# Optimization experiments

Measured on AMD Instinct MI355X. Metric: run time of the kernel, lower is better.

The kernel has to match this reference:

```python
import jax, jax.numpy as jnp
import numpy as np
import math

B, C, T = 4, 512, 2048
LN_EPS = 1e-5

def setup_inputs() -> dict:
    key = jax.random.key(0)
    ks = jax.random.split(key, 12)
    s = 1.0 / math.sqrt(C)
    inp = {
        'feat': jax.random.normal(ks[0], (B, C, T), dtype=jnp.float32),
        'Wq': jax.random.normal(ks[1], (C, C), dtype=jnp.float32) * s,
        'bq': jax.random.normal(ks[2], (C,), dtype=jnp.float32) * s,
        'Wk': jax.random.normal(ks[3], (C, C), dtype=jnp.float32) * s,
        'bk': jax.random.normal(ks[4], (C,), dtype=jnp.float32) * s,
        'Wv': jax.random.normal(ks[5], (C, C), dtype=jnp.float32) * s,
        'bv': jax.random.normal(ks[6], (C,), dtype=jnp.float32) * s,
        'Ws': jax.random.normal(ks[7], (C, C), dtype=jnp.float32) * s,
        'bs': jax.random.normal(ks[8], (C,), dtype=jnp.float32) * s,
        'Wl': jax.random.normal(ks[9], (C,), dtype=jnp.float32) * s,
        'bl': jax.random.normal(ks[10], (1,), dtype=jnp.float32) * s,
    }
    return inp

def reference(feat, Wq, bq, Wk, bk, Wv, bv, Ws, bs, Wl, bl):
    d = feat.shape[1]
    # 1x1 Conv1d == per-position linear over channels. feat: [B,C,T]
    value = jnp.einsum('oc,bct->bto', Wv, feat) + bv          # [B,T,C]
    query = jnp.einsum('oc,bct->bto', Wq, feat) + bq          # [B,T,C]
    key_  = jnp.einsum('oc,bct->bct', Wk, feat) + bk[:, None] # [B,C,T]
    f = jnp.einsum('btc,bcs->bts', query, key_) / math.sqrt(d)
    f = jax.nn.softmax(f, axis=2)                             # [B,T,T]
    y = jnp.einsum('bts,bsc->btc', f, value)                  # [B,T,C]
    f_score = jax.nn.sigmoid(jnp.einsum('btc,c->bt', y, Wl) + bl[0])
    z = jnp.einsum('bts,bsc->btc', 1.0 - f, value)            # [B,T,C]
    b_score = 1.0 - jax.nn.sigmoid(jnp.einsum('btc,c->bt', z, Wl) + bl[0])
    f_score = (f_score + b_score) / 2.0
    y_ct = jnp.einsum('oc,btc->bot', Ws, y) + bs[:, None]     # smooth conv, [B,C,T]
    out = feat + y_ct
    # LayerNorm over (C, T) jointly, default affine (weight=1, bias=0)
    mu = jnp.mean(out, axis=(1, 2), keepdims=True)
    var = jnp.mean(jnp.square(out - mu), axis=(1, 2), keepdims=True)
    out = (out - mu) * jax.lax.rsqrt(var + LN_EPS)
    return out, f_score
```

## Files before the change

kernel.cpp:

```cpp
#include <hip/hip_runtime.h>
#include <hip/hip_bf16.h>

#define BB 4
#define CC 512
#define TT 2048
static constexpr long CT  = (long)CC * TT;
static constexpr long TC  = (long)TT * CC;
static constexpr long TTT = (long)TT * TT;
static constexpr float SM_SCALE = 0.04419417382415922f;

typedef __bf16 bf16;
typedef __attribute__((ext_vector_type(8))) __bf16 bf16x8;
typedef __attribute__((ext_vector_type(4))) __bf16 bf16x4;
typedef __attribute__((ext_vector_type(4))) float f32x4;

__device__ __forceinline__ void load_lds16(const bf16* g, bf16* l)
{
    __builtin_amdgcn_global_load_lds(
        (const __attribute__((address_space(1))) void*)g,
        (__attribute__((address_space(3))) void*)l, 16, 0, 0);
}

template <int TM, int TN, int WR, int WC, int BK>
struct Core {
    static constexpr int THREADS = WR * WC * 64;
    static constexpr int MI = TM / (WR * 16);
    static constexpr int NI = TN / (WC * 16);
    static constexpr int CPR = BK / 8;
    static constexpr int RSH = (BK == 64) ? 3 : 2;
    static constexpr int CMASK = CPR - 1;
    static constexpr int CHUNKS = (TM + TN) * CPR;
    static constexpr int ACH = TM * CPR;
    static constexpr int CPT = CHUNKS / THREADS;
    static_assert(CPT * THREADS == CHUNKS, "chunk divisibility");

    __device__ static __forceinline__ void run(
        const bf16* __restrict__ Ab, const bf16* __restrict__ Bb,
        int K, int m0, int n0, bf16* As, bf16* Bs, f32x4 (&acc)[MI][NI])
    {
        const int tid  = threadIdx.x;
        const int lane = tid & 63;
        const int wid  = tid >> 6;
        const int wr = (wid / WC) * (MI * 16);
        const int wc = (wid % WC) * (NI * 16);
        const int lm = lane & 15;
        const int lq = lane >> 4;
        for (int k0 = 0; k0 < K; k0 += BK) {
#pragma unroll
            for (int i = 0; i < CPT; ++i) {
                int c = tid + i * THREADS;
                if (c < ACH) {
                    int row = c >> RSH;
                    int gc  = (c & CMASK) ^ (row & CMASK);
                    load_lds16(Ab + (long)(m0 + row) * K + k0 + gc * 8, As + c * 8);
                } else {
                    int d = c - ACH;
                    int row = d >> RSH;
                    int gc  = (d & CMASK) ^ (row & CMASK);
                    load_lds16(Bb + (long)(n0 + row) * K + k0 + gc * 8, Bs + d * 8);
                }
            }
            __syncthreads();
#pragma unroll
            for (int ks = 0; ks < BK / 32; ++ks) {
                bf16x8 af[MI], bfr[NI];
#pragma unroll
                for (int i = 0; i < MI; ++i) {
                    int ar = wr + i * 16 + lm;
                    int cc = (ks * 4 + lq) ^ (ar & CMASK);
                    af[i] = *(const bf16x8*)(As + ar * BK + cc * 8);
                }
#pragma unroll
                for (int i = 0; i < NI; ++i) {
                    int br = wc + i * 16 + lm;
                    int cc = (ks * 4 + lq) ^ (br & CMASK);
                    bfr[i] = *(const bf16x8*)(Bs + br * BK + cc * 8);
                }
#pragma unroll
                for (int mi = 0; mi < MI; ++mi)
#pragma unroll
                    for (int ni = 0; ni < NI; ++ni)
                        acc[mi][ni] = __builtin_amdgcn_mfma_f32_16x16x32_bf16(
                            af[mi], bfr[ni], acc[mi][ni], 0, 0, 0);
            }
            __syncthreads();
        }
    }
};

struct CoreQV {
    static constexpr int THREADS = 512;
    static constexpr int MI = 2;
    static constexpr int NI = 4;
    static constexpr int BK = 64;
    static constexpr int CPR = 8, RSH = 3, CMASK = 7;
    static constexpr int ACH = 128 * 8;
    static constexpr int CHUNKS = 256 * 8;
    static constexpr int CPT = CHUNKS / THREADS;

    __device__ static __forceinline__ void run(
        const bf16* __restrict__ Ab, const bf16* __restrict__ Bq,
        const bf16* __restrict__ Bv,
        int m0, bf16* As, bf16* Bs, f32x4 (&acc)[MI][NI])
    {
        const int tid  = threadIdx.x;
        const int lane = tid & 63;
        const int wid  = tid >> 6;
        const int wr = (wid / 2) * 32;
        const int wc = (wid % 2) * 64;
        const int lm = lane & 15;
        const int lq = lane >> 4;
        for (int k0 = 0; k0 < 512; k0 += BK) {
#pragma unroll
            for (int i = 0; i < CPT; ++i) {
                int c = tid + i * THREADS;
                if (c < ACH) {
                    int row = c >> RSH;
                    int gc  = (c & CMASK) ^ (row & CMASK);
                    load_lds16(Ab + (long)(m0 + row) * 512 + k0 + gc * 8, As + c * 8);
                } else {
                    int d = c - ACH;
                    int row = d >> RSH;
                    int gc  = (d & CMASK) ^ (row & CMASK);
                    const bf16* src = (row < 64)
                        ? Bq + (long)row * 512
                        : Bv + (long)(row - 64) * 512;
                    load_lds16(src + k0 + gc * 8, Bs + d * 8);
                }
            }
            __syncthreads();
#pragma unroll
            for (int ks = 0; ks < 2; ++ks) {
                bf16x8 af[MI], bfr[NI];
#pragma unroll
                for (int i = 0; i < MI; ++i) {
                    int ar = wr + i * 16 + lm;
                    int cc = (ks * 4 + lq) ^ (ar & CMASK);
                    af[i] = *(const bf16x8*)(As + ar * BK + cc * 8);
                }
#pragma unroll
                for (int i = 0; i < NI; ++i) {
                    int br = wc + i * 16 + lm;
                    int cc = (ks * 4 + lq) ^ (br & CMASK);
                    bfr[i] = *(const bf16x8*)(Bs + br * BK + cc * 8);
                }
#pragma unroll
                for (int mi = 0; mi < MI; ++mi)
#pragma unroll
                    for (int ni = 0; ni < NI; ++ni)
                        acc[mi][ni] = __builtin_amdgcn_mfma_f32_16x16x32_bf16(
                            af[mi], bfr[ni], acc[mi][ni], 0, 0, 0);
            }
            __syncthreads();
        }
    }
};

__global__ __launch_bounds__(512)
void gemm_qv_kernel(const bf16* __restrict__ featT, const bf16* __restrict__ Wq_bf,
                    const bf16* __restrict__ Wv_bf, bf16* __restrict__ Qb,
                    bf16* __restrict__ Vt, const float* __restrict__ bq,
                    const float* __restrict__ bv, const float* __restrict__ wkc,
                    const float* __restrict__ bk, float* __restrict__ qb)
{
    __shared__ bf16 As[128 * 64];
    __shared__ bf16 Bs[128 * 64];
    const int rb = blockIdx.z;
    const int m0 = blockIdx.y * 128;
    const int ng = blockIdx.x;
    const long wofs = (long)(ng * 64) * 512;
    f32x4 acc[2][4] = {};
    CoreQV::run(featT + (long)rb * TC, Wq_bf + wofs, Wv_bf + wofs, m0, As, Bs, acc);

    const int lane = threadIdx.x & 63, wid = threadIdx.x >> 6;
    const int wr = (wid / 2) * 32;
    const bool isV = wid & 1;
    const int lm = lane & 15, lq = lane >> 4;

    if (isV) {
        bf16* outV = Vt + (long)rb * CT;
#pragma unroll
        for (int mi = 0; mi < 2; ++mi)
#pragma unroll
            for (int ni = 0; ni < 4; ++ni) {
                int n = ng * 64 + ni * 16 + lm;
                float bn = bv[n];
                int mb = m0 + wr + mi * 16 + lq * 4;
                bf16x4 pk;
#pragma unroll
                for (int r = 0; r < 4; ++r) pk[r] = (bf16)(acc[mi][ni][r] + bn);
                *(bf16x4*)(outV + (long)n * TT + mb) = pk;
            }
    } else {
        bf16* out = Qb + (long)rb * TC;
        float* qbb = qb + (long)rb * TT;
        float rs[2][4] = {};
#pragma unroll
        for (int mi = 0; mi < 2; ++mi)
#pragma unroll
            for (int ni = 0; ni < 4; ++ni) {
                int n = ng * 64 + ni * 16 + lm;
                float bn = bq[n], wn = wkc[n], kn = bk[n];
#pragma unroll
                for (int r = 0; r < 4; ++r) {
                    int m = m0 + wr + mi * 16 + lq * 4 + r;
                    float v = acc[mi][ni][r] + bn;
                    rs[mi][r] += v * kn;
                    out[(long)m * 512 + n] = (bf16)(v * wn);
                }
            }
#pragma unroll
        for (int mi = 0; mi < 2; ++mi)
#pragma unroll
            for (int r = 0; r < 4; ++r) {
                float s = rs[mi][r];
                s += __shfl_xor(s, 1, 64); s += __shfl_xor(s, 2, 64);
                s += __shfl_xor(s, 4, 64); s += __shfl_xor(s, 8, 64);
                if (lm == 0)
                    atomicAdd(qbb + m0 + wr + mi * 16 + lq * 4 + r, s);
            }
    }
}

using CS = Core<128, 128, 4, 2, 64>;
__global__ __launch_bounds__(512)
void gemm_s_kernel(const bf16* __restrict__ Qb, const bf16* __restrict__ featT,
                   bf16* __restrict__ S, const float* __restrict__ qb,
                   float* __restrict__ rsum)
{
    __shared__ bf16 As[128 * 64];
    __shared__ bf16 Bs[128 * 64];
    const int id = blockIdx.x;
    const int xcd = id & 7, s = id >> 3;
    const int bz = xcd >> 1;
    const int n0 = (s & 15) * 128;
    const int m0 = (((xcd & 1) << 3) + (s >> 4)) * 128;
    f32x4 acc[CS::MI][CS::NI] = {};
    CS::run(Qb + (long)bz * TC, featT + (long)bz * TC, 512, m0, n0, As, Bs, acc);

    const int lane = threadIdx.x & 63, wid = threadIdx.x >> 6;
    const int wr = (wid >> 1) * 32, wc = (wid & 1) * 64;
    const int lm = lane & 15, lq = lane >> 4;
    bf16* out = S + (long)bz * TTT;
    const float* qbb = qb + (long)bz * TT;
    float* rsb = rsum + (long)bz * TT;
    float rp[2][4] = {};
#pragma unroll
    for (int mi = 0; mi < 2; ++mi)
#pragma unroll
        for (int ni = 0; ni < 4; ++ni)
#pragma unroll
            for (int r = 0; r < 4; ++r) {
                int m = m0 + wr + mi * 16 + lq * 4 + r;
                int n = n0 + wc + ni * 16 + lm;
                float p = __expf((acc[mi][ni][r] + qbb[m]) * SM_SCALE);
                out[(long)m * 2048 + n] = (bf16)p;
                rp[mi][r] += p;
            }
#pragma unroll
    for (int mi = 0; mi < 2; ++mi)
#pragma unroll
        for (int r = 0; r < 4; ++r) {
            float s2 = rp[mi][r];
            s2 += __shfl_xor(s2, 1, 64); s2 += __shfl_xor(s2, 2, 64);
            s2 += __shfl_xor(s2, 4, 64); s2 += __shfl_xor(s2, 8, 64);
            if (lm == 0)
                atomicAdd(rsb + m0 + wr + mi * 16 + lq * 4 + r, s2);
        }
}

using CY = Core<128, 64, 4, 2, 64>;
__global__ __launch_bounds__(512)
void gemm_y_kernel(const bf16* __restrict__ S, const bf16* __restrict__ Vt,
                   bf16* __restrict__ Yb, const float* __restrict__ Wl,
                   const float* __restrict__ rsum, float* __restrict__ u)
{
    __shared__ bf16 As[128 * 64];
    __shared__ bf16 Bs[64 * 64];
    const int id = blockIdx.x;
    const int xcd = id & 7, s = id >> 3;
    const int rb = xcd >> 1;
    const int n0 = (s & 7) * 64;
    const int m0 = (((xcd & 1) << 3) + (s >> 3)) * 128;
    f32x4 acc[CY::MI][CY::NI] = {};
    CY::run(S + (long)rb * TTT, Vt + (long)rb * CT, 2048, m0, n0, As, Bs, acc);

    const int lane = threadIdx.x & 63, wid = threadIdx.x >> 6;
    const int wr = (wid / 2) * 32, wc = (wid % 2) * 32;
    const int lm = lane & 15, lq = lane >> 4;
    bf16* out = Yb + (long)rb * TC;
    const float* rsb = rsum + (long)rb * TT;
    float* ub = u + (long)rb * TT;
    float inv[2][4];
#pragma unroll
    for (int mi = 0; mi < 2; ++mi)
#pragma unroll
        for (int r = 0; r < 4; ++r)
            inv[mi][r] = 1.f / rsb[m0 + wr + mi * 16 + lq * 4 + r];
    float rs[2][4] = {};
#pragma unroll
    for (int mi = 0; mi < 2; ++mi)
#pragma unroll
        for (int ni = 0; ni < 2; ++ni) {
            int n = n0 + wc + ni * 16 + lm;
            float wn = Wl[n];
#pragma unroll
            for (int r = 0; r < 4; ++r) {
                int m = m0 + wr + mi * 16 + lq * 4 + r;
                float v = acc[mi][ni][r] * inv[mi][r];
                out[(long)m * 512 + n] = (bf16)v;
                rs[mi][r] += v * wn;
            }
        }
#pragma unroll
    for (int mi = 0; mi < 2; ++mi)
#pragma unroll
        for (int r = 0; r < 4; ++r) {
            float s2 = rs[mi][r];
            s2 += __shfl_xor(s2, 1, 64); s2 += __shfl_xor(s2, 2, 64);
            s2 += __shfl_xor(s2, 4, 64); s2 += __shfl_xor(s2, 8, 64);
            if (lm == 0)
                atomicAdd(ub + m0 + wr + mi * 16 + lq * 4 + r, s2);
        }
}

using CF = Core<128, 64, 4, 2, 64>;
__global__ __launch_bounds__(512)
void gemm_final_kernel(const bf16* __restrict__ Yb, const bf16* __restrict__ Ws_bf,
                       float* __restrict__ out, const float* __restrict__ bs,
                       const float* __restrict__ feat, double* __restrict__ stats)
{
    __shared__ bf16 As[128 * 64];
    __shared__ bf16 Bs[64 * 64];
    __shared__ float red[16];
    const int id = blockIdx.x;
    const int xcd = id & 7, s = id >> 3;
    const int bz = xcd >> 1;
    const int n0 = (s & 7) * 64;
    const int m0 = (((xcd & 1) << 3) + (s >> 3)) * 128;
    f32x4 acc[CF::MI][CF::NI] = {};
    CF::run(Yb + (long)bz * TC, Ws_bf, 512, m0, n0, As, Bs, acc);

    const int tid = threadIdx.x;
    const int lane = tid & 63, wid = tid >> 6;
    const int wr = (wid / 2) * 32, wc = (wid % 2) * 32;
    const int lm = lane & 15, lq = lane >> 4;
    float s1 = 0.f, s2 = 0.f;
#pragma unroll
    for (int mi = 0; mi < 2; ++mi)
#pragma unroll
        for (int ni = 0; ni < 2; ++ni) {
            int mbase = m0 + wr + mi * 16 + lq * 4;
            int n = n0 + wc + ni * 16 + lm;
            long off = (long)bz * CT + (long)n * TT + mbase;
            f32x4 fv = *(const f32x4*)(feat + off);
            float bn = bs[n];
            f32x4 res;
#pragma unroll
            for (int r = 0; r < 4; ++r) {
                float v = acc[mi][ni][r] + bn + fv[r];
                res[r] = v;
                s1 += v;
                s2 += v * v;
            }
            *(f32x4*)(out + off) = res;
        }
#pragma unroll
    for (int off = 32; off; off >>= 1) {
        s1 += __shfl_xor(s1, off, 64);
        s2 += __shfl_xor(s2, off, 64);
    }
    if (lane == 0) { red[wid] = s1; red[8 + wid] = s2; }
    __syncthreads();
    if (tid == 0) {
        double t1 = 0.0, t2 = 0.0;
#pragma unroll
        for (int w = 0; w < 8; ++w) { t1 += red[w]; t2 += red[8 + w]; }
        atomicAdd(stats + bz * 2, t1);
        atomicAdd(stats + bz * 2 + 1, t2);
    }
}

__global__ __launch_bounds__(256)
void prep_kernel(const float* __restrict__ feat, bf16* __restrict__ featT,
                 const float* __restrict__ Wq, const float* __restrict__ Wv,
                 const float* __restrict__ Ws, bf16* __restrict__ Wbf,
                 const float* __restrict__ Wk, const float* __restrict__ Wl,
                 const float* __restrict__ bv, float* __restrict__ wkc,
                 float* __restrict__ wvl, float* __restrict__ wlbv,
                 float* __restrict__ frp, float* __restrict__ qb,
                 float* __restrict__ u, float* __restrict__ rsum,
                 double* __restrict__ stats)
{
    const int blk = blockIdx.x;
    const int tid = threadIdx.x;
    if (blk < 4096) {
        __shared__ float tile[32][33];
        __shared__ float sfr[4][32];
        const int b  = blk >> 10;
        const int c0 = ((blk & 1023) >> 6) * 32;
        const int tt = blk & 63;
        const int t0 = tt * 32;
        const int tx = tid & 31;
        const int ty = tid >> 5;
#pragma unroll
        for (int j = 0; j < 4; ++j) {
            int c = c0 + ty + j * 8;
            tile[ty + j * 8][tx] = feat[(long)b * CT + (long)c * TT + t0 + tx];
        }
        __syncthreads();
        float ps = 0.f;
#pragma unroll
        for (int j = 0; j < 4; ++j) {
            int tl = ty + j * 8;
            int t = t0 + tl;
            int c = c0 + tx;
            float v = tile[tx][tl];
            ps += v;
            featT[(long)b * TC + (long)t * CC + c] = (bf16)v;
        }
        const int wid = tid >> 6;
        ps += __shfl_xor(ps, 32, 64);
        if ((tid & 63) < 32) sfr[wid][tx] = ps;
        __syncthreads();
        if (tid < 32) {
            float s = sfr[0][tid] + sfr[1][tid] + sfr[2][tid] + sfr[3][tid];
            frp[(((long)b * 64 + tt) << 9) + c0 + tid] = s;
        }
    } else if (blk < 4480) {
        long gid = (long)(blk - 4096) * 256 + tid;
        long idx = gid * 8;
        int w = (int)(idx >> 18);
        long off = idx & 262143;
        const float* src = (w == 0) ? Wq : (w == 1) ? Wv : Ws;
        f32x4 a = *(const f32x4*)(src + off);
        f32x4 b = *(const f32x4*)(src + off + 4);
        bf16x8 o;
#pragma unroll
        for (int j = 0; j < 4; ++j) { o[j] = (bf16)a[j]; o[4 + j] = (bf16)b[j]; }
        *(bf16x8*)(Wbf + idx) = o;
    } else {
        int mid = (blk - 4480) * 256 + tid;
        if (mid < 512) {
            float s = 0.f;
            for (int o = 0; o < 512; ++o) s += Wk[o * 512 + mid];
            wkc[mid] = s;
        } else if (mid < 1024) {
            int k = mid - 512;
            float s = 0.f;
            for (int c = 0; c < 512; ++c) s += Wl[c] * Wv[c * 512 + k];
            wvl[k] = s;
        } else if (mid < 1088) {
            int lane = mid - 1024;
            float s = 0.f;
#pragma unroll
            for (int j = 0; j < 8; ++j) s += Wl[lane + 64 * j] * bv[lane + 64 * j];
#pragma unroll
            for (int off = 32; off; off >>= 1) s += __shfl_xor(s, off, 64);
            if (lane == 0) wlbv[0] = s;
        } else if (mid >= 1152 && mid < 1160) {
            stats[mid - 1152] = 0.0;
        } else if (mid >= 4096 && mid < 12288) {
            qb[mid - 4096] = 0.f;
        } else if (mid >= 12288 && mid < 20480) {
            u[mid - 12288] = 0.f;
        } else if (mid >= 20480 && mid < 28672) {
            rsum[mid - 20480] = 0.f;
        }
    }
}

__global__ __launch_bounds__(256)
void ln_score_kernel(float* __restrict__ out, const double* __restrict__ stats,
                     const float* __restrict__ u, const float* __restrict__ frp,
                     const float* __restrict__ wvl, const float* __restrict__ wlbv,
                     const float* __restrict__ blp)
{
    if (blockIdx.x < 4096) {
        long i = ((long)blockIdx.x * 256 + threadIdx.x) * 4;
        int b = (int)(i >> 20);
        const double n = 1048576.0;
        double mu  = stats[b * 2] / n;
        double var = stats[b * 2 + 1] / n - mu * mu;
        float rs = (float)(1.0 / sqrt(var + 1e-5));
        float muf = (float)mu;
        f32x4 v = *(f32x4*)(out + i);
#pragma unroll
        for (int j = 0; j < 4; ++j) v[j] = (v[j] - muf) * rs;
        *(f32x4*)(out + i) = v;
    } else {
        const int b = blockIdx.x - 4096;
        __shared__ float ssv[4];
        const int tid = threadIdx.x, lane = tid & 63, wid = tid >> 6;
        const float* fb = frp + ((long)b * 64 << 9);
        float s0 = 0.f, s1 = 0.f;
#pragma unroll 8
        for (int k = 0; k < 64; ++k) {
            s0 += fb[(k << 9) + tid];
            s1 += fb[(k << 9) + tid + 256];
        }
        float p = s0 * wvl[tid] + s1 * wvl[tid + 256];
#pragma unroll
        for (int off = 32; off; off >>= 1) p += __shfl_xor(p, off, 64);
        if (lane == 0) ssv[wid] = p;
        __syncthreads();
        const float sv = ssv[0] + ssv[1] + ssv[2] + ssv[3] + 2048.f * wlbv[0];
        const float bl0 = blp[0];
#pragma unroll
        for (int j = 0; j < 8; ++j) {
            int t = tid + j * 256;
            float uu = u[(long)b * TT + t];
            float uf = uu + bl0;
            float vf = sv - uu + bl0;
            float fs  = 1.f / (1.f + __expf(-uf));
            float bsc = 1.f - 1.f / (1.f + __expf(-vf));
            out[(long)BB * CT + (long)b * TT + t] = 0.5f * (fs + bsc);
        }
    }
}

extern "C" void kernel_launch(void* const* d_in, const int* in_sizes, int n_in,
                              void* d_out, int out_size, void* d_ws, size_t ws_size,
                              hipStream_t stream)
{
    const float* feat = (const float*)d_in[0];
    const float* Wq   = (const float*)d_in[1];
    const float* bq   = (const float*)d_in[2];
    const float* Wk   = (const float*)d_in[3];
    const float* bk   = (const float*)d_in[4];
    const float* Wv   = (const float*)d_in[5];
    const float* bv   = (const float*)d_in[6];
    const float* Ws   = (const float*)d_in[7];
    const float* bs   = (const float*)d_in[8];
    const float* Wl   = (const float*)d_in[9];
    const float* bl   = (const float*)d_in[10];
    float* out = (float*)d_out;

    if (ws_size < 69316736) return;
    char* ws = (char*)d_ws;
    bf16* featT  = (bf16*)(ws);
    bf16* Wbf    = (bf16*)(ws + 8388608);
    bf16* Qb     = (bf16*)(ws + 9961472);
    bf16* Vt     = (bf16*)(ws + 18350080);
    bf16* Yb     = (bf16*)(ws + 26738688);
    bf16* S      = (bf16*)(ws + 35127296);
    float* wkc   = (float*)(ws + 68689920);
    float* wvl   = (float*)(ws + 68691968);
    float* wlbv  = (float*)(ws + 68694016);
    float* qb    = (float*)(ws + 68694080);
    double* stats= (double*)(ws + 68726848);
    float* u     = (float*)(ws + 68726912);
    float* rsum  = (float*)(ws + 68759680);
    float* frp   = (float*)(ws + 68792448);

    bf16* Wq_bf = Wbf;
    bf16* Wv_bf = Wbf + 262144;
    bf16* Ws_bf = Wbf + 524288;

    prep_kernel<<<4592, 256, 0, stream>>>(feat, featT, Wq, Wv, Ws, Wbf, Wk, Wl, bv,
                                          wkc, wvl, wlbv, frp, qb, u, rsum, stats);
    gemm_qv_kernel<<<dim3(8, 16, 4), 512, 0, stream>>>(
        featT, Wq_bf, Wv_bf, Qb, Vt, bq, bv, wkc, bk, qb);
    gemm_s_kernel<<<1024, 512, 0, stream>>>(Qb, featT, S, qb, rsum);
    gemm_y_kernel<<<512, 512, 0, stream>>>(S, Vt, Yb, Wl, rsum, u);
    gemm_final_kernel<<<512, 512, 0, stream>>>(Yb, Ws_bf, out, bs, feat, stats);
    ln_score_kernel<<<4100, 256, 0, stream>>>(out, stats, u, frp, wvl, wlbv, bl);
}
```

Before: 224.2 us.

## Rewrite score GEMM as 256x256 tile with half-tile staged LDS pipeline

Result: no change. 220.5 us (-1.7%).

```diff
diff --git a/kernel.cpp b/kernel.cpp
--- a/kernel.cpp
+++ b/kernel.cpp
@@ -222,51 +222,128 @@
     }
 }
 
-using CS = Core<128, 128, 4, 2, 64>;
-__global__ __launch_bounds__(512)
-void gemm_s_kernel(const bf16* __restrict__ Qb, const bf16* __restrict__ featT,
-                   bf16* __restrict__ S, const float* __restrict__ qb,
-                   float* __restrict__ rsum)
-{
-    __shared__ bf16 As[128 * 64];
-    __shared__ bf16 Bs[128 * 64];
-    const int id = blockIdx.x;
-    const int xcd = id & 7, s = id >> 3;
-    const int bz = xcd >> 1;
-    const int n0 = (s & 15) * 128;
-    const int m0 = (((xcd & 1) << 3) + (s >> 4)) * 128;
-    f32x4 acc[CS::MI][CS::NI] = {};
-    CS::run(Qb + (long)bz * TC, featT + (long)bz * TC, 512, m0, n0, As, Bs, acc);
-
-    const int lane = threadIdx.x & 63, wid = threadIdx.x >> 6;
-    const int wr = (wid >> 1) * 32, wc = (wid & 1) * 64;
+__global__ __launch_bounds__(512, 2)
+void gemm_s256_kernel(const bf16* __restrict__ Qb, const bf16* __restrict__ featT,
+                      bf16* __restrict__ S, const float* __restrict__ qb,
+                      float* __restrict__ rsum)
+{
+    __shared__ __align__(16) bf16 lds[2][2][256 * 64];
+    const int id   = blockIdx.x;
+    const int xcd  = id & 7, sIdx = id >> 3;
+    const int bz   = xcd >> 1;
+    const int n0   = (sIdx & 7) * 256;
+    const int m0   = (((xcd & 1) << 2) + (sIdx >> 3)) * 256;
+    const bf16* __restrict__ Ab = Qb + (long)bz * TC;
+    const bf16* __restrict__ Bb = featT + (long)bz * TC;
+
+    const int tid  = threadIdx.x;
+    const int lane = tid & 63;
+    const int wid  = tid >> 6;
     const int lm = lane & 15, lq = lane >> 4;
-    bf16* out = S + (long)bz * TTT;
+    const int wrb = (wid >> 2) * 64;
+    const int wcb = (wid & 3) * 32;
+
+    f32x4 acc[8][4] = {};
+
+#define FENCE asm volatile("" ::: "memory")
+
+#define STAGE_HT(t, op, h)                                                    \
+    do {                                                                      \
+        const bf16* gp_ = (op) ? Bb : Ab;                                     \
+        const int  br_  = ((op) ? n0 : m0) + (h) * 128;                       \
+        bf16* lp_ = &lds[(t) & 1][op][(h) * 128 * 64];                        \
+        _Pragma("unroll")                                                     \
+        for (int i_ = 0; i_ < 2; ++i_) {                                      \
+            int c_ = tid + i_ * 512;                                          \
+            int r_ = c_ >> 3;                                                 \
+            int g_ = (c_ & 7) ^ (r_ & 7);                                     \
+            load_lds16(gp_ + (long)(br_ + r_) * 512 + (t) * 64 + g_ * 8,      \
+                       lp_ + c_ * 8);                                         \
+        }                                                                     \
+    } while (0)
+
+#define PHASE(t, qm, qn, doSt, st, sop, sh, doVm)                             \
+    do {                                                                      \
+        bf16x8 af[2][4], bfr[2][2];                                           \
+        const bf16* Al_ = lds[(t) & 1][0];                                    \
+        const bf16* Bl_ = lds[(t) & 1][1];                                    \
+        _Pragma("unroll")                                                     \
+        for (int ks = 0; ks < 2; ++ks) {                                      \
+            _Pragma("unroll")                                                 \
+            for (int j = 0; j < 4; ++j) {                                     \
+                int ar = (qm) * 128 + wrb + j * 16 + lm;                      \
+                int cc = (ks * 4 + lq) ^ (ar & 7);                            \
+                af[ks][j] = *(const bf16x8*)(Al_ + ar * 64 + cc * 8);         \
+            }                                                                 \
+            _Pragma("unroll")                                                 \
+            for (int j = 0; j < 2; ++j) {                                     \
+                int br = (qn) * 128 + wcb + j * 16 + lm;                      \
+                int cc = (ks * 4 + lq) ^ (br & 7);                            \
+                bfr[ks][j] = *(const bf16x8*)(Bl_ + br * 64 + cc * 8);        \
+            }                                                                 \
+        }                                                                     \
+        if (doSt) STAGE_HT(st, sop, sh);                                      \
+        if (doVm) {                                                           \
+            if ((t) < 6) asm volatile("s_waitcnt vmcnt(4)" ::: "memory");     \
+            else         asm volatile("s_waitcnt vmcnt(0)" ::: "memory");     \
+        }                                                                     \
+        FENCE; __builtin_amdgcn_s_barrier(); FENCE;                           \
+        __builtin_amdgcn_s_setprio(1);                                        \
+        _Pragma("unroll")                                                     \
+        for (int ks = 0; ks < 2; ++ks)                                        \
+            _Pragma("unroll")                                                 \
+            for (int j = 0; j < 4; ++j)                                       \
+                _Pragma("unroll")                                             \
+                for (int j2 = 0; j2 < 2; ++j2)                                \
+                    acc[(qm) * 4 + j][(qn) * 2 + j2] =                        \
+                        __builtin_amdgcn_mfma_f32_16x16x32_bf16(              \
+                            af[ks][j], bfr[ks][j2],                           \
+                            acc[(qm) * 4 + j][(qn) * 2 + j2], 0, 0, 0);       \
+        __builtin_amdgcn_s_setprio(0);                                        \
+        FENCE; __builtin_amdgcn_s_barrier(); FENCE;                           \
+    } while (0)
+
+    STAGE_HT(0, 0, 0); STAGE_HT(0, 1, 0); STAGE_HT(0, 0, 1); STAGE_HT(0, 1, 1);
+    STAGE_HT(1, 0, 0); STAGE_HT(1, 1, 0);
+    asm volatile("s_waitcnt vmcnt(4)" ::: "memory");
+    FENCE; __builtin_amdgcn_s_barrier(); FENCE;
+
+    for (int t = 0; t < 8; ++t) {
+        PHASE(t, 0, 0, t + 1 < 8, t + 1, 0, 1, false);
+        PHASE(t, 0, 1, t + 1 < 8, t + 1, 1, 1, false);
+        PHASE(t, 1, 0, t + 2 < 8, t + 2, 0, 0, false);
+        PHASE(t, 1, 1, t + 2 < 8, t + 2, 1, 0, true);
+    }
+#undef PHASE
+#undef STAGE_HT
+#undef FENCE
+
+    bf16* outp = S + (long)bz * TTT;
     const float* qbb = qb + (long)bz * TT;
     float* rsb = rsum + (long)bz * TT;
-    float rp[2][4] = {};
-#pragma unroll
-    for (int mi = 0; mi < 2; ++mi)
-#pragma unroll
-        for (int ni = 0; ni < 4; ++ni)
+#pragma unroll
+    for (int mi = 0; mi < 8; ++mi) {
+        const int mrow = m0 + (mi >> 2) * 128 + wrb + (mi & 3) * 16 + lq * 4;
+        const f32x4 qv = *(const f32x4*)(qbb + mrow);
+        float rp[4] = {0.f, 0.f, 0.f, 0.f};
+#pragma unroll
+        for (int ni = 0; ni < 4; ++ni) {
+            const int ncol = n0 + (ni >> 1) * 128 + wcb + (ni & 1) * 16 + lm;
 #pragma unroll
             for (int r = 0; r < 4; ++r) {
-                int m = m0 + wr + mi * 16 + lq * 4 + r;
-                int n = n0 + wc + ni * 16 + lm;
-                float p = __expf((acc[mi][ni][r] + qbb[m]) * SM_SCALE);
-                out[(long)m * 2048 + n] = (bf16)p;
-                rp[mi][r] += p;
-            }
-#pragma unroll
-    for (int mi = 0; mi < 2; ++mi)
+                float p = __expf((acc[mi][ni][r] + qv[r]) * SM_SCALE);
+                outp[(long)(mrow + r) * 2048 + ncol] = (bf16)p;
+                rp[r] += p;
+            }
+        }
 #pragma unroll
         for (int r = 0; r < 4; ++r) {
-            float s2 = rp[mi][r];
+            float s2 = rp[r];
             s2 += __shfl_xor(s2, 1, 64); s2 += __shfl_xor(s2, 2, 64);
             s2 += __shfl_xor(s2, 4, 64); s2 += __shfl_xor(s2, 8, 64);
-            if (lm == 0)
-                atomicAdd(rsb + m0 + wr + mi * 16 + lq * 4 + r, s2);
-        }
+            if (lm == 0) atomicAdd(rsb + mrow + r, s2);
+        }
+    }
 }
 
 using CY = Core<128, 64, 4, 2, 64>;
@@ -561,7 +638,7 @@
                                           wkc, wvl, wlbv, frp, qb, u, rsum, stats);
     gemm_qv_kernel<<<dim3(8, 16, 4), 512, 0, stream>>>(
         featT, Wq_bf, Wv_bf, Qb, Vt, bq, bv, wkc, bk, qb);
-    gemm_s_kernel<<<1024, 512, 0, stream>>>(Qb, featT, S, qb, rsum);
+    gemm_s256_kernel<<<256, 512, 0, stream>>>(Qb, featT, S, qb, rsum);
     gemm_y_kernel<<<512, 512, 0, stream>>>(S, Vt, Yb, Wl, rsum, u);
     gemm_final_kernel<<<512, 512, 0, stream>>>(Yb, Ws_bf, out, bs, feat, stats);
     ln_score_kernel<<<4100, 256, 0, stream>>>(out, stats, u, frp, wvl, wlbv, bl);
```
